# Performance work log

Measured on AMD Instinct MI355X. Metric: run time of the kernel, lower is better.

Reference implementation:

```python
import jax, jax.numpy as jnp
import numpy as np

H = 512  # hidden_dim


def setup_inputs() -> dict:
    key = jax.random.key(0)
    k1, k2, k3 = jax.random.split(key, 3)
    context = jax.random.normal(k1, (32, 512, H), dtype=jnp.float32)
    query = jax.random.normal(k2, (32, 64, H), dtype=jnp.float32)
    # similarity_linear.weight has shape (1, 3H); store flattened as (3H,)
    W = jax.random.normal(k3, (3 * H,), dtype=jnp.float32) * (1.0 / np.sqrt(3 * H))
    return {"context": context, "query": query, "W": W}


def reference(context, query, W):
    # Decompose W into the three blocks applied to [c, q, c*q].
    w_c, w_q, w_m = W[:H], W[H:2 * H], W[2 * H:]
    # S[b,i,j] = c_i.w_c + q_j.w_q + sum_d c_id * q_jd * w_m_d  -- same math as
    # Linear(3H,1) over cat([c_exp, q_exp, c_exp*q_exp]), without the O(B*C*Q*3H) tensor.
    s_c = context @ w_c                       # [B, C]
    s_q = query @ w_q                         # [B, Q]
    s_m = jnp.einsum('bcd,bqd->bcq', context * w_m, query)  # [B, C, Q]
    S = s_m + s_c[:, :, None] + s_q[:, None, :]              # [B, C, Q]

    a = jax.nn.softmax(S, axis=2)             # context-to-query attention
    attended_query = jnp.einsum('bcq,bqd->bcd', a, query)    # [B, C, H]

    b = jax.nn.softmax(jnp.max(S, axis=2), axis=1)           # [B, C]
    attended_context = jnp.einsum('bc,bcd->bd', b, context)  # [B, H]
    attended_context = jnp.broadcast_to(attended_context[:, None, :], context.shape)

    G = jnp.concatenate([
        context,
        attended_query,
        context * attended_query,
        context * attended_context,
    ], axis=2)  # [B, C, 4H]
    return G
```

## Files before the change

kernel.cpp:

```cpp
#include <hip/hip_runtime.h>
#include <cstdint>

#define NB 32
#define NC 512
#define NQ 64
#define ND 512

typedef __attribute__((ext_vector_type(8))) short bf16x8;
typedef __attribute__((ext_vector_type(8))) short short8;
typedef __attribute__((ext_vector_type(4))) float f32x4;

__device__ __forceinline__ short f2bf(float f) {
  union { float f; unsigned u; } v; v.f = f;
  v.u += 0x7fffu + ((v.u >> 16) & 1u);
  return (short)(v.u >> 16);
}

#define PITCH 72
#define P_OFF  0
#define CM_OFF 4608
#define QQ_OFF 9216
#define SCS_F  6912
#define SQS_F  6976
#define PML_F  7040
#define PEL_F  7168
#define AQF_F  7296
#define AQP    68
#define SM_SHORTS 23296

__device__ __forceinline__ int qswz(int dd) {
  return (((dd & 7) ^ ((dd >> 3) & 7)) * 8);
}

__global__ __launch_bounds__(512) void k1_main(
    const float* __restrict__ ctx, const float* __restrict__ qry,
    const float* __restrict__ W, float* __restrict__ G, float* __restrict__ m_ws)
{
  __shared__ __align__(16) short sm[SM_SHORTS];
  float* smf = (float*)sm;

  const int t    = threadIdx.x;
  const int lane = t & 63;
  const int w    = t >> 6;
  const int ln15 = lane & 15;
  const int g    = lane >> 4;
  const int cw   = (w >> 1) * 16;
  const int qh   = w & 1;
  const int qw   = qh * 32;
  const int b    = blockIdx.x >> 3;
  const int c0   = (blockIdx.x & 7) * 64;

  const int lr = t >> 3;
  const int j8 = (t & 7) * 8;

  f32x4 acc[2] = {};
  float scp = 0.f, sqp = 0.f;

  for (int kc = 0; kc < 8; ++kc) {
    const int d0 = kc * 64;
    __syncthreads();
    {
      const float* crow = ctx + ((size_t)(b*NC + c0 + lr))*ND + d0 + j8;
      const float4 ca = *(const float4*)(crow);
      const float4 cb = *(const float4*)(crow + 4);
      const float4 wca = *(const float4*)(W + d0 + j8);
      const float4 wcb = *(const float4*)(W + d0 + j8 + 4);
      const float4 wma = *(const float4*)(W + 2*ND + d0 + j8);
      const float4 wmb = *(const float4*)(W + 2*ND + d0 + j8 + 4);
      scp += ca.x*wca.x + ca.y*wca.y + ca.z*wca.z + ca.w*wca.w
           + cb.x*wcb.x + cb.y*wcb.y + cb.z*wcb.z + cb.w*wcb.w;
      short8 cs;
      cs[0]=f2bf(ca.x*wma.x); cs[1]=f2bf(ca.y*wma.y); cs[2]=f2bf(ca.z*wma.z); cs[3]=f2bf(ca.w*wma.w);
      cs[4]=f2bf(cb.x*wmb.x); cs[5]=f2bf(cb.y*wmb.y); cs[6]=f2bf(cb.z*wmb.z); cs[7]=f2bf(cb.w*wmb.w);
      *(short8*)&sm[CM_OFF + lr*PITCH + j8] = cs;
    }
    {
      const float* qrow = qry + ((size_t)(b*NQ + lr))*ND + d0 + j8;
      const float4 qa = *(const float4*)(qrow);
      const float4 qb = *(const float4*)(qrow + 4);
      const float4 wqa = *(const float4*)(W + ND + d0 + j8);
      const float4 wqb = *(const float4*)(W + ND + d0 + j8 + 4);
      sqp += qa.x*wqa.x + qa.y*wqa.y + qa.z*wqa.z + qa.w*wqa.w
           + qb.x*wqb.x + qb.y*wqb.y + qb.z*wqb.z + qb.w*wqb.w;
      short8 qs;
      qs[0]=f2bf(qa.x); qs[1]=f2bf(qa.y); qs[2]=f2bf(qa.z); qs[3]=f2bf(qa.w);
      qs[4]=f2bf(qb.x); qs[5]=f2bf(qb.y); qs[6]=f2bf(qb.z); qs[7]=f2bf(qb.w);
      *(short8*)&sm[QQ_OFF + lr*PITCH + j8] = qs;
    }
    __syncthreads();
    #pragma unroll
    for (int kk = 0; kk < 2; ++kk) {
      const bf16x8 a = *(const bf16x8*)&sm[CM_OFF + (cw + ln15)*PITCH + kk*32 + g*8];
      #pragma unroll
      for (int n = 0; n < 2; ++n) {
        const bf16x8 bq = *(const bf16x8*)&sm[QQ_OFF + (qw + n*16 + ln15)*PITCH + kk*32 + g*8];
        acc[n] = __builtin_amdgcn_mfma_f32_16x16x32_bf16(a, bq, acc[n], 0, 0, 0);
      }
    }
  }

  scp += __shfl_xor(scp, 1, 8); scp += __shfl_xor(scp, 2, 8); scp += __shfl_xor(scp, 4, 8);
  sqp += __shfl_xor(sqp, 1, 8); sqp += __shfl_xor(sqp, 2, 8); sqp += __shfl_xor(sqp, 4, 8);
  if ((t & 7) == 0) { smf[SCS_F + lr] = scp; smf[SQS_F + lr] = sqp; }
  __syncthreads();

  float ev0[4], ev1[4], pmr[4];
  #pragma unroll
  for (int reg = 0; reg < 4; ++reg) {
    float sv0 = acc[0][reg] + smf[SQS_F + qw + ln15];
    float sv1 = acc[1][reg] + smf[SQS_F + qw + 16 + ln15];
    float pm = fmaxf(sv0, sv1);
    pm = fmaxf(pm, __shfl_xor(pm, 1, 16));
    pm = fmaxf(pm, __shfl_xor(pm, 2, 16));
    pm = fmaxf(pm, __shfl_xor(pm, 4, 16));
    pm = fmaxf(pm, __shfl_xor(pm, 8, 16));
    const float e0 = __expf(sv0 - pm), e1 = __expf(sv1 - pm);
    float pe = e0 + e1;
    pe += __shfl_xor(pe, 1, 16); pe += __shfl_xor(pe, 2, 16);
    pe += __shfl_xor(pe, 4, 16); pe += __shfl_xor(pe, 8, 16);
    ev0[reg] = e0; ev1[reg] = e1; pmr[reg] = pm;
    if (ln15 == 0) { smf[PML_F + qh*64 + cw + g*4 + reg] = pm;
                     smf[PEL_F + qh*64 + cw + g*4 + reg] = pe; }
  }
  __syncthreads();

  #pragma unroll
  for (int reg = 0; reg < 4; ++reg) {
    const int rloc = cw + g*4 + reg;
    const float m0 = smf[PML_F + rloc], m1 = smf[PML_F + 64 + rloc];
    const float s0 = smf[PEL_F + rloc], s1 = smf[PEL_F + 64 + rloc];
    const float M  = fmaxf(m0, m1);
    const float S  = s0*__expf(m0 - M) + s1*__expf(m1 - M);
    const float f  = __expf(pmr[reg] - M) / S;
    if (qh == 0 && ln15 == 0) m_ws[b*NC + c0 + rloc] = M + smf[SCS_F + rloc];
    sm[P_OFF + rloc*PITCH + qw + ln15]      = f2bf(ev0[reg] * f);
    sm[P_OFF + rloc*PITCH + qw + 16 + ln15] = f2bf(ev1[reg] * f);
  }
  __syncthreads();

  bf16x8 pa[2];
  pa[0] = *(const bf16x8*)&sm[P_OFF + (cw + ln15)*PITCH + g*8];
  pa[1] = *(const bf16x8*)&sm[P_OFF + (cw + ln15)*PITCH + 32 + g*8];

  const int sr = t >> 4, sc = (t & 15) * 4;

  for (int dc = 0; dc < 8; ++dc) {
    const int d0 = dc * 64;
    __syncthreads();
    {
      const float* qrow = qry + ((size_t)(b*NQ + lr))*ND + d0 + j8;
      const float4 a0 = *(const float4*)(qrow);
      const float4 a1 = *(const float4*)(qrow + 4);
      const float e[8] = {a0.x,a0.y,a0.z,a0.w,a1.x,a1.y,a1.z,a1.w};
      #pragma unroll
      for (int v = 0; v < 8; ++v) {
        const int dd = j8 + v;
        sm[CM_OFF + dd*PITCH + (lr ^ qswz(dd))] = f2bf(e[v]);
      }
    }
    __syncthreads();
    f32x4 acc2[2] = {};
    #pragma unroll
    for (int kk = 0; kk < 2; ++kk)
      #pragma unroll
      for (int n = 0; n < 2; ++n) {
        const int dd = qw + n*16 + ln15;
        const bf16x8 bq = *(const bf16x8*)&sm[CM_OFF + dd*PITCH + ((kk*32 + g*8) ^ qswz(dd))];
        acc2[n] = __builtin_amdgcn_mfma_f32_16x16x32_bf16(pa[kk], bq, acc2[n], 0, 0, 0);
      }
    #pragma unroll
    for (int n = 0; n < 2; ++n)
      #pragma unroll
      for (int reg = 0; reg < 4; ++reg)
        smf[AQF_F + (cw + g*4 + reg)*AQP + qw + n*16 + ln15] = acc2[n][reg];
    __syncthreads();
    #pragma unroll
    for (int k4 = 0; k4 < 2; ++k4) {
      const int r = k4*32 + sr;
      const float4 aq4 = *(const float4*)&smf[AQF_F + r*AQP + sc];
      const float4 cv  = *(const float4*)(ctx + ((size_t)(b*NC + c0 + r))*ND + d0 + sc);
      float* gp = G + ((size_t)(b*NC + c0 + r))*2048 + d0 + sc;
      *(float4*)(gp)        = cv;
      *(float4*)(gp + 512)  = aq4;
      *(float4*)(gp + 1024) = make_float4(cv.x*aq4.x, cv.y*aq4.y,
                                          cv.z*aq4.z, cv.w*aq4.w);
    }
  }
}

__global__ __launch_bounds__(256) void k2_partial(
    const float* __restrict__ ctx, const float* __restrict__ m_ws, float* __restrict__ pc)
{
  const int t  = threadIdx.x;
  const int b  = blockIdx.x >> 4;
  const int ch = blockIdx.x & 15;
  __shared__ float r8[8];
  __shared__ float wts[32];

  const float v0 = m_ws[b*NC + t];
  const float v1 = m_ws[b*NC + 256 + t];
  float mx = fmaxf(v0, v1);
  #pragma unroll
  for (int o = 32; o; o >>= 1) mx = fmaxf(mx, __shfl_xor(mx, o, 64));
  if ((t & 63) == 0) r8[t >> 6] = mx;
  __syncthreads();
  mx = fmaxf(fmaxf(r8[0], r8[1]), fmaxf(r8[2], r8[3]));
  float e = __expf(v0 - mx) + __expf(v1 - mx);
  #pragma unroll
  for (int o = 32; o; o >>= 1) e += __shfl_xor(e, o, 64);
  if ((t & 63) == 0) r8[4 + (t >> 6)] = e;
  __syncthreads();
  const float denom = r8[4] + r8[5] + r8[6] + r8[7];
  if (t < 32) wts[t] = __expf(m_ws[b*NC + ch*32 + t] - mx) / denom;
  __syncthreads();

  float s0 = 0.f, s1 = 0.f;
  const float* base = ctx + ((size_t)(b*NC + ch*32))*ND;
  for (int c = 0; c < 32; ++c) {
    const float w = wts[c];
    s0 += w * base[(size_t)c*ND + t];
    s1 += w * base[(size_t)c*ND + t + 256];
  }
  pc[((size_t)(b*16 + ch))*ND + t]       = s0;
  pc[((size_t)(b*16 + ch))*ND + t + 256] = s1;
}

__global__ __launch_bounds__(512) void k2_reduce(
    const float* __restrict__ pc, float* __restrict__ ac)
{
  const int b = blockIdx.x;
  const int d = threadIdx.x;
  float s = 0.f;
  #pragma unroll
  for (int ch = 0; ch < 16; ++ch) s += pc[((size_t)(b*16 + ch))*ND + d];
  ac[b*ND + d] = s;
}

__global__ __launch_bounds__(256) void k3_part3(
    const float* __restrict__ ctx, const float* __restrict__ ac, float* __restrict__ G)
{
  const size_t e = ((size_t)blockIdx.x*256 + threadIdx.x) * 8;
  const int b = (int)(e >> 18);
  const int r = (int)(e & 262143);
  const int c = r >> 9;
  const int d = r & 511;
  const float4 x0 = *(const float4*)(ctx + e);
  const float4 x1 = *(const float4*)(ctx + e + 4);
  const float4 a0 = *(const float4*)(ac + b*ND + d);
  const float4 a1 = *(const float4*)(ac + b*ND + d + 4);
  float* gp = G + ((size_t)(b*NC + c))*2048 + 1536 + d;
  *(float4*)(gp)     = make_float4(x0.x*a0.x, x0.y*a0.y, x0.z*a0.z, x0.w*a0.w);
  *(float4*)(gp + 4) = make_float4(x1.x*a1.x, x1.y*a1.y, x1.z*a1.z, x1.w*a1.w);
}

extern "C" void kernel_launch(void* const* d_in, const int* in_sizes, int n_in,
                              void* d_out, int out_size, void* d_ws, size_t ws_size,
                              hipStream_t stream)
{
  const float* ctx = (const float*)d_in[0];
  const float* qry = (const float*)d_in[1];
  const float* W   = (const float*)d_in[2];
  float* G = (float*)d_out;

  float* m_ws = (float*)d_ws;
  float* pc   = m_ws + NB*NC;
  float* ac   = pc + (size_t)NB*16*ND;

  k1_main   <<<dim3(NB*8),  dim3(512), 0, stream>>>(ctx, qry, W, G, m_ws);
  k2_partial<<<dim3(NB*16), dim3(256), 0, stream>>>(ctx, m_ws, pc);
  k2_reduce <<<dim3(NB),    dim3(512), 0, stream>>>(pc, ac);
  k3_part3  <<<dim3((NB*NC*ND)/(256*8)), dim3(256), 0, stream>>>(ctx, ac, G);
}
```

Before: 65.00 us.

## Widen d-chunks to 128, write context slice early, store attended query as bf16

The chunk width in both the score loop and the attended-query loop doubles from 64 to 128, which halves the number of iterations and barriers. The block index is swizzled across batches. The first G slice (context copy) is now written during the score phase from the context values already loaded. The attended-query staging buffer in shared memory becomes bf16, so the epilogue reads fewer bytes and G's attended-query part now carries bf16 precision. This cuts synchronization and duplicate global context loads for the copy, but adds precision loss and register pressure.

```diff
diff --git a/kernel.cpp b/kernel.cpp
--- a/kernel.cpp
+++ b/kernel.cpp
@@ -15,17 +15,20 @@
   v.u += 0x7fffu + ((v.u >> 16) & 1u);
   return (short)(v.u >> 16);
 }
-
-#define PITCH 72
-#define P_OFF  0
-#define CM_OFF 4608
-#define QQ_OFF 9216
-#define SCS_F  6912
-#define SQS_F  6976
-#define PML_F  7040
-#define PEL_F  7168
-#define AQF_F  7296
-#define AQP    68
+__device__ __forceinline__ float bf2f(short s) {
+  union { float f; unsigned u; } v; v.u = ((unsigned)(unsigned short)s) << 16;
+  return v.f;
+}
+
+#define P_OFF   0
+#define CM_OFF  4608
+#define QQ_OFF  13312
+#define QT_OFF  4608
+#define AQB_OFF 13824
+#define SCS_F   11264
+#define SQS_F   11328
+#define PML_F   11392
+#define PEL_F   11520
 #define SM_SHORTS 23296
 
 __device__ __forceinline__ int qswz(int dd) {
@@ -47,53 +50,74 @@
   const int cw   = (w >> 1) * 16;
   const int qh   = w & 1;
   const int qw   = qh * 32;
-  const int b    = blockIdx.x >> 3;
-  const int c0   = (blockIdx.x & 7) * 64;
-
-  const int lr = t >> 3;
-  const int j8 = (t & 7) * 8;
+  const int bid  = (int)blockIdx.x;
+  const int swz  = (bid & 7) * 32 + (bid >> 3);
+  const int b    = swz >> 3;
+  const int c0   = (swz & 7) * 64;
+
+  const int lr  = t >> 3;
+  const int j16 = (t & 7) * 16;
 
   f32x4 acc[2] = {};
   float scp = 0.f, sqp = 0.f;
 
-  for (int kc = 0; kc < 8; ++kc) {
-    const int d0 = kc * 64;
+  for (int kc = 0; kc < 4; ++kc) {
+    const int d0 = kc * 128;
     __syncthreads();
     {
-      const float* crow = ctx + ((size_t)(b*NC + c0 + lr))*ND + d0 + j8;
-      const float4 ca = *(const float4*)(crow);
-      const float4 cb = *(const float4*)(crow + 4);
-      const float4 wca = *(const float4*)(W + d0 + j8);
-      const float4 wcb = *(const float4*)(W + d0 + j8 + 4);
-      const float4 wma = *(const float4*)(W + 2*ND + d0 + j8);
-      const float4 wmb = *(const float4*)(W + 2*ND + d0 + j8 + 4);
-      scp += ca.x*wca.x + ca.y*wca.y + ca.z*wca.z + ca.w*wca.w
-           + cb.x*wcb.x + cb.y*wcb.y + cb.z*wcb.z + cb.w*wcb.w;
-      short8 cs;
-      cs[0]=f2bf(ca.x*wma.x); cs[1]=f2bf(ca.y*wma.y); cs[2]=f2bf(ca.z*wma.z); cs[3]=f2bf(ca.w*wma.w);
-      cs[4]=f2bf(cb.x*wmb.x); cs[5]=f2bf(cb.y*wmb.y); cs[6]=f2bf(cb.z*wmb.z); cs[7]=f2bf(cb.w*wmb.w);
-      *(short8*)&sm[CM_OFF + lr*PITCH + j8] = cs;
+      const float* crow = ctx + ((size_t)(b*NC + c0 + lr))*ND + d0 + j16;
+      float4 cv0 = ((const float4*)crow)[0], cv1 = ((const float4*)crow)[1];
+      float4 cv2 = ((const float4*)crow)[2], cv3 = ((const float4*)crow)[3];
+      const float4 wc0 = *(const float4*)(W + d0 + j16);
+      const float4 wc1 = *(const float4*)(W + d0 + j16 + 4);
+      const float4 wc2 = *(const float4*)(W + d0 + j16 + 8);
+      const float4 wc3 = *(const float4*)(W + d0 + j16 + 12);
+      const float4 wm0 = *(const float4*)(W + 2*ND + d0 + j16);
+      const float4 wm1 = *(const float4*)(W + 2*ND + d0 + j16 + 4);
+      const float4 wm2 = *(const float4*)(W + 2*ND + d0 + j16 + 8);
+      const float4 wm3 = *(const float4*)(W + 2*ND + d0 + j16 + 12);
+      scp += cv0.x*wc0.x + cv0.y*wc0.y + cv0.z*wc0.z + cv0.w*wc0.w
+           + cv1.x*wc1.x + cv1.y*wc1.y + cv1.z*wc1.z + cv1.w*wc1.w
+           + cv2.x*wc2.x + cv2.y*wc2.y + cv2.z*wc2.z + cv2.w*wc2.w
+           + cv3.x*wc3.x + cv3.y*wc3.y + cv3.z*wc3.z + cv3.w*wc3.w;
+      short8 s0, s1;
+      s0[0]=f2bf(cv0.x*wm0.x); s0[1]=f2bf(cv0.y*wm0.y); s0[2]=f2bf(cv0.z*wm0.z); s0[3]=f2bf(cv0.w*wm0.w);
+      s0[4]=f2bf(cv1.x*wm1.x); s0[5]=f2bf(cv1.y*wm1.y); s0[6]=f2bf(cv1.z*wm1.z); s0[7]=f2bf(cv1.w*wm1.w);
+      s1[0]=f2bf(cv2.x*wm2.x); s1[1]=f2bf(cv2.y*wm2.y); s1[2]=f2bf(cv2.z*wm2.z); s1[3]=f2bf(cv2.w*wm2.w);
+      s1[4]=f2bf(cv3.x*wm3.x); s1[5]=f2bf(cv3.y*wm3.y); s1[6]=f2bf(cv3.z*wm3.z); s1[7]=f2bf(cv3.w*wm3.w);
+      *(short8*)&sm[CM_OFF + lr*136 + j16]     = s0;
+      *(short8*)&sm[CM_OFF + lr*136 + j16 + 8] = s1;
+      float* gp0 = G + ((size_t)(b*NC + c0 + lr))*2048 + d0 + j16;
+      ((float4*)gp0)[0] = cv0; ((float4*)gp0)[1] = cv1;
+      ((float4*)gp0)[2] = cv2; ((float4*)gp0)[3] = cv3;
     }
     {
-      const float* qrow = qry + ((size_t)(b*NQ + lr))*ND + d0 + j8;
-      const float4 qa = *(const float4*)(qrow);
-      const float4 qb = *(const float4*)(qrow + 4);
-      const float4 wqa = *(const float4*)(W + ND + d0 + j8);
-      const float4 wqb = *(const float4*)(W + ND + d0 + j8 + 4);
-      sqp += qa.x*wqa.x + qa.y*wqa.y + qa.z*wqa.z + qa.w*wqa.w
-           + qb.x*wqb.x + qb.y*wqb.y + qb.z*wqb.z + qb.w*wqb.w;
-      short8 qs;
-      qs[0]=f2bf(qa.x); qs[1]=f2bf(qa.y); qs[2]=f2bf(qa.z); qs[3]=f2bf(qa.w);
-      qs[4]=f2bf(qb.x); qs[5]=f2bf(qb.y); qs[6]=f2bf(qb.z); qs[7]=f2bf(qb.w);
-      *(short8*)&sm[QQ_OFF + lr*PITCH + j8] = qs;
+      const float* qrow = qry + ((size_t)(b*NQ + lr))*ND + d0 + j16;
+      float4 qv0 = ((const float4*)qrow)[0], qv1 = ((const float4*)qrow)[1];
+      float4 qv2 = ((const float4*)qrow)[2], qv3 = ((const float4*)qrow)[3];
+      const float4 wq0 = *(const float4*)(W + ND + d0 + j16);
+      const float4 wq1 = *(const float4*)(W + ND + d0 + j16 + 4);
+      const float4 wq2 = *(const float4*)(W + ND + d0 + j16 + 8);
+      const float4 wq3 = *(const float4*)(W + ND + d0 + j16 + 12);
+      sqp += qv0.x*wq0.x + qv0.y*wq0.y + qv0.z*wq0.z + qv0.w*wq0.w
+           + qv1.x*wq1.x + qv1.y*wq1.y + qv1.z*wq1.z + qv1.w*wq1.w
+           + qv2.x*wq2.x + qv2.y*wq2.y + qv2.z*wq2.z + qv2.w*wq2.w
+           + qv3.x*wq3.x + qv3.y*wq3.y + qv3.z*wq3.z + qv3.w*wq3.w;
+      short8 s0, s1;
+      s0[0]=f2bf(qv0.x); s0[1]=f2bf(qv0.y); s0[2]=f2bf(qv0.z); s0[3]=f2bf(qv0.w);
+      s0[4]=f2bf(qv1.x); s0[5]=f2bf(qv1.y); s0[6]=f2bf(qv1.z); s0[7]=f2bf(qv1.w);
+      s1[0]=f2bf(qv2.x); s1[1]=f2bf(qv2.y); s1[2]=f2bf(qv2.z); s1[3]=f2bf(qv2.w);
+      s1[4]=f2bf(qv3.x); s1[5]=f2bf(qv3.y); s1[6]=f2bf(qv3.z); s1[7]=f2bf(qv3.w);
+      *(short8*)&sm[QQ_OFF + lr*136 + j16]     = s0;
+      *(short8*)&sm[QQ_OFF + lr*136 + j16 + 8] = s1;
     }
     __syncthreads();
     #pragma unroll
-    for (int kk = 0; kk < 2; ++kk) {
-      const bf16x8 a = *(const bf16x8*)&sm[CM_OFF + (cw + ln15)*PITCH + kk*32 + g*8];
+    for (int kk = 0; kk < 4; ++kk) {
+      const bf16x8 a = *(const bf16x8*)&sm[CM_OFF + (cw + ln15)*136 + kk*32 + g*8];
       #pragma unroll
       for (int n = 0; n < 2; ++n) {
-        const bf16x8 bq = *(const bf16x8*)&sm[QQ_OFF + (qw + n*16 + ln15)*PITCH + kk*32 + g*8];
+        const bf16x8 bq = *(const bf16x8*)&sm[QQ_OFF + (qw + n*16 + ln15)*136 + kk*32 + g*8];
         acc[n] = __builtin_amdgcn_mfma_f32_16x16x32_bf16(a, bq, acc[n], 0, 0, 0);
       }
     }
@@ -133,57 +157,68 @@
     const float S  = s0*__expf(m0 - M) + s1*__expf(m1 - M);
     const float f  = __expf(pmr[reg] - M) / S;
     if (qh == 0 && ln15 == 0) m_ws[b*NC + c0 + rloc] = M + smf[SCS_F + rloc];
-    sm[P_OFF + rloc*PITCH + qw + ln15]      = f2bf(ev0[reg] * f);
-    sm[P_OFF + rloc*PITCH + qw + 16 + ln15] = f2bf(ev1[reg] * f);
+    sm[P_OFF + rloc*72 + qw + ln15]      = f2bf(ev0[reg] * f);
+    sm[P_OFF + rloc*72 + qw + 16 + ln15] = f2bf(ev1[reg] * f);
   }
   __syncthreads();
 
   bf16x8 pa[2];
-  pa[0] = *(const bf16x8*)&sm[P_OFF + (cw + ln15)*PITCH + g*8];
-  pa[1] = *(const bf16x8*)&sm[P_OFF + (cw + ln15)*PITCH + 32 + g*8];
-
-  const int sr = t >> 4, sc = (t & 15) * 4;
-
-  for (int dc = 0; dc < 8; ++dc) {
-    const int d0 = dc * 64;
+  pa[0] = *(const bf16x8*)&sm[P_OFF + (cw + ln15)*72 + g*8];
+  pa[1] = *(const bf16x8*)&sm[P_OFF + (cw + ln15)*72 + 32 + g*8];
+
+  const int dh = qh;
+
+  for (int dc = 0; dc < 4; ++dc) {
+    const int d0 = dc * 128;
     __syncthreads();
     {
-      const float* qrow = qry + ((size_t)(b*NQ + lr))*ND + d0 + j8;
-      const float4 a0 = *(const float4*)(qrow);
-      const float4 a1 = *(const float4*)(qrow + 4);
-      const float e[8] = {a0.x,a0.y,a0.z,a0.w,a1.x,a1.y,a1.z,a1.w};
-      #pragma unroll
-      for (int v = 0; v < 8; ++v) {
-        const int dd = j8 + v;
-        sm[CM_OFF + dd*PITCH + (lr ^ qswz(dd))] = f2bf(e[v]);
+      const float* qrow = qry + ((size_t)(b*NQ + lr))*ND + d0 + j16;
+      const float4 a0 = ((const float4*)qrow)[0];
+      const float4 a1 = ((const float4*)qrow)[1];
+      const float4 a2 = ((const float4*)qrow)[2];
+      const float4 a3 = ((const float4*)qrow)[3];
+      const float e[16] = {a0.x,a0.y,a0.z,a0.w, a1.x,a1.y,a1.z,a1.w,
+                           a2.x,a2.y,a2.z,a2.w, a3.x,a3.y,a3.z,a3.w};
+      #pragma unroll
+      for (int v = 0; v < 16; ++v) {
+        const int dd = j16 + v;
+        sm[QT_OFF + dd*72 + (lr ^ qswz(dd))] = f2bf(e[v]);
       }
     }
     __syncthreads();
-    f32x4 acc2[2] = {};
+    f32x4 acc2[4] = {};
     #pragma unroll
     for (int kk = 0; kk < 2; ++kk)
       #pragma unroll
-      for (int n = 0; n < 2; ++n) {
-        const int dd = qw + n*16 + ln15;
-        const bf16x8 bq = *(const bf16x8*)&sm[CM_OFF + dd*PITCH + ((kk*32 + g*8) ^ qswz(dd))];
+      for (int n = 0; n < 4; ++n) {
+        const int dd = dh*64 + n*16 + ln15;
+        const bf16x8 bq = *(const bf16x8*)&sm[QT_OFF + dd*72 + ((kk*32 + g*8) ^ qswz(dd))];
         acc2[n] = __builtin_amdgcn_mfma_f32_16x16x32_bf16(pa[kk], bq, acc2[n], 0, 0, 0);
       }
     #pragma unroll
-    for (int n = 0; n < 2; ++n)
+    for (int n = 0; n < 4; ++n)
       #pragma unroll
       for (int reg = 0; reg < 4; ++reg)
-        smf[AQF_F + (cw + g*4 + reg)*AQP + qw + n*16 + ln15] = acc2[n][reg];
-    __syncthreads();
-    #pragma unroll
-    for (int k4 = 0; k4 < 2; ++k4) {
-      const int r = k4*32 + sr;
-      const float4 aq4 = *(const float4*)&smf[AQF_F + r*AQP + sc];
-      const float4 cv  = *(const float4*)(ctx + ((size_t)(b*NC + c0 + r))*ND + d0 + sc);
-      float* gp = G + ((size_t)(b*NC + c0 + r))*2048 + d0 + sc;
-      *(float4*)(gp)        = cv;
-      *(float4*)(gp + 512)  = aq4;
-      *(float4*)(gp + 1024) = make_float4(cv.x*aq4.x, cv.y*aq4.y,
-                                          cv.z*aq4.z, cv.w*aq4.w);
+        sm[AQB_OFF + (cw + g*4 + reg)*136 + dh*64 + n*16 + ln15] = f2bf(acc2[n][reg]);
+    __syncthreads();
+    {
+      const short8 ab0 = *(const short8*)&sm[AQB_OFF + lr*136 + j16];
+      const short8 ab1 = *(const short8*)&sm[AQB_OFF + lr*136 + j16 + 8];
+      float aq[16];
+      #pragma unroll
+      for (int i = 0; i < 8; ++i) { aq[i] = bf2f(ab0[i]); aq[8+i] = bf2f(ab1[i]); }
+      const float* crow = ctx + ((size_t)(b*NC + c0 + lr))*ND + d0 + j16;
+      float4 cv0 = ((const float4*)crow)[0], cv1 = ((const float4*)crow)[1];
+      float4 cv2 = ((const float4*)crow)[2], cv3 = ((const float4*)crow)[3];
+      float* gp = G + ((size_t)(b*NC + c0 + lr))*2048 + d0 + j16;
+      ((float4*)(gp + 512))[0] = make_float4(aq[0], aq[1], aq[2], aq[3]);
+      ((float4*)(gp + 512))[1] = make_float4(aq[4], aq[5], aq[6], aq[7]);
+      ((float4*)(gp + 512))[2] = make_float4(aq[8], aq[9], aq[10], aq[11]);
+      ((float4*)(gp + 512))[3] = make_float4(aq[12], aq[13], aq[14], aq[15]);
+      ((float4*)(gp + 1024))[0] = make_float4(cv0.x*aq[0], cv0.y*aq[1], cv0.z*aq[2], cv0.w*aq[3]);
+      ((float4*)(gp + 1024))[1] = make_float4(cv1.x*aq[4], cv1.y*aq[5], cv1.z*aq[6], cv1.w*aq[7]);
+      ((float4*)(gp + 1024))[2] = make_float4(cv2.x*aq[8], cv2.y*aq[9], cv2.z*aq[10], cv2.w*aq[11]);
+      ((float4*)(gp + 1024))[3] = make_float4(cv3.x*aq[12], cv3.y*aq[13], cv3.z*aq[14], cv3.w*aq[15]);
     }
   }
 }
```

After: 79.99 us. +23.1%, slower.

## Split score/softmax from output pass, fuse all four G blocks in one kernel

Applied to the files above, without the earlier changes.

Restructures the pipeline so one kernel computes scores and the softmax probabilities and writes them in bf16 to workspace. A prep kernel transposes query to bf16 once per batch, and a new output kernel does the P·Q matmul and writes all four G segments in one pass. This removes the separate part-3 kernel, which re-read context, and the per-chunk query transpose inside the main loop. It adds the round-trips for P and transposed Q, and rounds attended_query to bf16 before storing, which loses precision. Kernel A and kernel B each use 256 threads and 32 context rows per block.

```diff
diff --git a/kernel.cpp b/kernel.cpp
--- a/kernel.cpp
+++ b/kernel.cpp
@@ -15,28 +15,54 @@
   v.u += 0x7fffu + ((v.u >> 16) & 1u);
   return (short)(v.u >> 16);
 }
-
-#define PITCH 72
-#define P_OFF  0
-#define CM_OFF 4608
-#define QQ_OFF 9216
-#define SCS_F  6912
-#define SQS_F  6976
-#define PML_F  7040
-#define PEL_F  7168
-#define AQF_F  7296
-#define AQP    68
-#define SM_SHORTS 23296
-
-__device__ __forceinline__ int qswz(int dd) {
-  return (((dd & 7) ^ ((dd >> 3) & 7)) * 8);
-}
-
-__global__ __launch_bounds__(512) void k1_main(
+__device__ __forceinline__ float bf2f(short s) {
+  union { float f; unsigned u; } v; v.u = ((unsigned)(unsigned short)s) << 16;
+  return v.f;
+}
+
+__global__ __launch_bounds__(512) void kPrep(
+    const float* __restrict__ qry, short* __restrict__ qTbf)
+{
+  __shared__ short lq[NQ*ND];
+  const int b = blockIdx.x;
+  const int t = threadIdx.x;
+  const int r = t >> 3;
+  const int cb = (t & 7) * 64;
+  const float* qrow = qry + ((size_t)(b*NQ + r))*ND + cb;
+  #pragma unroll
+  for (int i = 0; i < 16; ++i) {
+    const float4 qv = *(const float4*)(qrow + i*4);
+    short4 s; s.x=f2bf(qv.x); s.y=f2bf(qv.y); s.z=f2bf(qv.z); s.w=f2bf(qv.w);
+    *(short4*)&lq[r*ND + cb + i*4] = s;
+  }
+  __syncthreads();
+  const int d = t;
+  short* qTrow = qTbf + ((size_t)(b*ND + d))*NQ;
+  #pragma unroll
+  for (int j = 0; j < 16; ++j) {
+    short4 h4;
+    h4.x = lq[(j*4+0)*ND + d];
+    h4.y = lq[(j*4+1)*ND + d];
+    h4.z = lq[(j*4+2)*ND + d];
+    h4.w = lq[(j*4+3)*ND + d];
+    *(short4*)&qTrow[j*4] = h4;
+  }
+}
+
+#define KA_CM 0
+#define KA_QQ 2304
+#define KA_P  6912
+#define KA_SCS 4608
+#define KA_SQS 4640
+#define KA_PML 4704
+#define KA_PEL 4768
+#define KA_SHORTS 9664
+
+__global__ __launch_bounds__(256) void kA(
     const float* __restrict__ ctx, const float* __restrict__ qry,
-    const float* __restrict__ W, float* __restrict__ G, float* __restrict__ m_ws)
-{
-  __shared__ __align__(16) short sm[SM_SHORTS];
+    const float* __restrict__ W, short* __restrict__ Pws, float* __restrict__ m_ws)
+{
+  __shared__ __align__(16) short sm[KA_SHORTS];
   float* smf = (float*)sm;
 
   const int t    = threadIdx.x;
@@ -47,11 +73,11 @@
   const int cw   = (w >> 1) * 16;
   const int qh   = w & 1;
   const int qw   = qh * 32;
-  const int b    = blockIdx.x >> 3;
-  const int c0   = (blockIdx.x & 7) * 64;
-
-  const int lr = t >> 3;
-  const int j8 = (t & 7) * 8;
+  const int b    = blockIdx.x >> 4;
+  const int c0   = (blockIdx.x & 15) * 32;
+
+  const int lr = t >> 3, j8  = (t & 7) * 8;
+  const int qr = t >> 2, i16 = (t & 3) * 16;
 
   f32x4 acc[2] = {};
   float scp = 0.f, sqp = 0.f;
@@ -72,43 +98,54 @@
       short8 cs;
       cs[0]=f2bf(ca.x*wma.x); cs[1]=f2bf(ca.y*wma.y); cs[2]=f2bf(ca.z*wma.z); cs[3]=f2bf(ca.w*wma.w);
       cs[4]=f2bf(cb.x*wmb.x); cs[5]=f2bf(cb.y*wmb.y); cs[6]=f2bf(cb.z*wmb.z); cs[7]=f2bf(cb.w*wmb.w);
-      *(short8*)&sm[CM_OFF + lr*PITCH + j8] = cs;
+      *(short8*)&sm[KA_CM + lr*72 + j8] = cs;
     }
     {
-      const float* qrow = qry + ((size_t)(b*NQ + lr))*ND + d0 + j8;
+      const float* qrow = qry + ((size_t)(b*NQ + qr))*ND + d0 + i16;
       const float4 qa = *(const float4*)(qrow);
       const float4 qb = *(const float4*)(qrow + 4);
-      const float4 wqa = *(const float4*)(W + ND + d0 + j8);
-      const float4 wqb = *(const float4*)(W + ND + d0 + j8 + 4);
-      sqp += qa.x*wqa.x + qa.y*wqa.y + qa.z*wqa.z + qa.w*wqa.w
-           + qb.x*wqb.x + qb.y*wqb.y + qb.z*wqb.z + qb.w*wqb.w;
-      short8 qs;
-      qs[0]=f2bf(qa.x); qs[1]=f2bf(qa.y); qs[2]=f2bf(qa.z); qs[3]=f2bf(qa.w);
-      qs[4]=f2bf(qb.x); qs[5]=f2bf(qb.y); qs[6]=f2bf(qb.z); qs[7]=f2bf(qb.w);
-      *(short8*)&sm[QQ_OFF + lr*PITCH + j8] = qs;
+      const float4 qc = *(const float4*)(qrow + 8);
+      const float4 qd = *(const float4*)(qrow + 12);
+      const float4 wa  = *(const float4*)(W + ND + d0 + i16);
+      const float4 wb  = *(const float4*)(W + ND + d0 + i16 + 4);
+      const float4 wc2 = *(const float4*)(W + ND + d0 + i16 + 8);
+      const float4 wd  = *(const float4*)(W + ND + d0 + i16 + 12);
+      sqp += qa.x*wa.x + qa.y*wa.y + qa.z*wa.z + qa.w*wa.w
+           + qb.x*wb.x + qb.y*wb.y + qb.z*wb.z + qb.w*wb.w
+           + qc.x*wc2.x + qc.y*wc2.y + qc.z*wc2.z + qc.w*wc2.w
+           + qd.x*wd.x + qd.y*wd.y + qd.z*wd.z + qd.w*wd.w;
+      short8 s1, s2;
+      s1[0]=f2bf(qa.x); s1[1]=f2bf(qa.y); s1[2]=f2bf(qa.z); s1[3]=f2bf(qa.w);
+      s1[4]=f2bf(qb.x); s1[5]=f2bf(qb.y); s1[6]=f2bf(qb.z); s1[7]=f2bf(qb.w);
+      s2[0]=f2bf(qc.x); s2[1]=f2bf(qc.y); s2[2]=f2bf(qc.z); s2[3]=f2bf(qc.w);
+      s2[4]=f2bf(qd.x); s2[5]=f2bf(qd.y); s2[6]=f2bf(qd.z); s2[7]=f2bf(qd.w);
+      *(short8*)&sm[KA_QQ + qr*72 + i16]     = s1;
+      *(short8*)&sm[KA_QQ + qr*72 + i16 + 8] = s2;
     }
     __syncthreads();
     #pragma unroll
     for (int kk = 0; kk < 2; ++kk) {
-      const bf16x8 a = *(const bf16x8*)&sm[CM_OFF + (cw + ln15)*PITCH + kk*32 + g*8];
+      const bf16x8 a = *(const bf16x8*)&sm[KA_CM + (cw + ln15)*72 + kk*32 + g*8];
       #pragma unroll
       for (int n = 0; n < 2; ++n) {
-        const bf16x8 bq = *(const bf16x8*)&sm[QQ_OFF + (qw + n*16 + ln15)*PITCH + kk*32 + g*8];
+        const bf16x8 bq = *(const bf16x8*)&sm[KA_QQ + (qw + n*16 + ln15)*72 + kk*32 + g*8];
         acc[n] = __builtin_amdgcn_mfma_f32_16x16x32_bf16(a, bq, acc[n], 0, 0, 0);
       }
     }
   }
 
   scp += __shfl_xor(scp, 1, 8); scp += __shfl_xor(scp, 2, 8); scp += __shfl_xor(scp, 4, 8);
-  sqp += __shfl_xor(sqp, 1, 8); sqp += __shfl_xor(sqp, 2, 8); sqp += __shfl_xor(sqp, 4, 8);
-  if ((t & 7) == 0) { smf[SCS_F + lr] = scp; smf[SQS_F + lr] = sqp; }
+  if ((t & 7) == 0) smf[KA_SCS + lr] = scp;
+  sqp += __shfl_xor(sqp, 1, 4); sqp += __shfl_xor(sqp, 2, 4);
+  if ((t & 3) == 0) smf[KA_SQS + qr] = sqp;
   __syncthreads();
 
   float ev0[4], ev1[4], pmr[4];
   #pragma unroll
   for (int reg = 0; reg < 4; ++reg) {
-    float sv0 = acc[0][reg] + smf[SQS_F + qw + ln15];
-    float sv1 = acc[1][reg] + smf[SQS_F + qw + 16 + ln15];
+    const int rloc = cw + g*4 + reg;
+    float sv0 = acc[0][reg] + smf[KA_SQS + qw + ln15];
+    float sv1 = acc[1][reg] + smf[KA_SQS + qw + 16 + ln15];
     float pm = fmaxf(sv0, sv1);
     pm = fmaxf(pm, __shfl_xor(pm, 1, 16));
     pm = fmaxf(pm, __shfl_xor(pm, 2, 16));
@@ -119,72 +156,29 @@
     pe += __shfl_xor(pe, 1, 16); pe += __shfl_xor(pe, 2, 16);
     pe += __shfl_xor(pe, 4, 16); pe += __shfl_xor(pe, 8, 16);
     ev0[reg] = e0; ev1[reg] = e1; pmr[reg] = pm;
-    if (ln15 == 0) { smf[PML_F + qh*64 + cw + g*4 + reg] = pm;
-                     smf[PEL_F + qh*64 + cw + g*4 + reg] = pe; }
+    if (ln15 == 0) { smf[KA_PML + qh*32 + rloc] = pm;
+                     smf[KA_PEL + qh*32 + rloc] = pe; }
   }
   __syncthreads();
 
   #pragma unroll
   for (int reg = 0; reg < 4; ++reg) {
     const int rloc = cw + g*4 + reg;
-    const float m0 = smf[PML_F + rloc], m1 = smf[PML_F + 64 + rloc];
-    const float s0 = smf[PEL_F + rloc], s1 = smf[PEL_F + 64 + rloc];
+    const float m0 = smf[KA_PML + rloc], m1 = smf[KA_PML + 32 + rloc];
+    const float s0 = smf[KA_PEL + rloc], s1 = smf[KA_PEL + 32 + rloc];
     const float M  = fmaxf(m0, m1);
     const float S  = s0*__expf(m0 - M) + s1*__expf(m1 - M);
     const float f  = __expf(pmr[reg] - M) / S;
-    if (qh == 0 && ln15 == 0) m_ws[b*NC + c0 + rloc] = M + smf[SCS_F + rloc];
-    sm[P_OFF + rloc*PITCH + qw + ln15]      = f2bf(ev0[reg] * f);
-    sm[P_OFF + rloc*PITCH + qw + 16 + ln15] = f2bf(ev1[reg] * f);
-  }
-  __syncthreads();
-
-  bf16x8 pa[2];
-  pa[0] = *(const bf16x8*)&sm[P_OFF + (cw + ln15)*PITCH + g*8];
-  pa[1] = *(const bf16x8*)&sm[P_OFF + (cw + ln15)*PITCH + 32 + g*8];
-
-  const int sr = t >> 4, sc = (t & 15) * 4;
-
-  for (int dc = 0; dc < 8; ++dc) {
-    const int d0 = dc * 64;
-    __syncthreads();
-    {
-      const float* qrow = qry + ((size_t)(b*NQ + lr))*ND + d0 + j8;
-      const float4 a0 = *(const float4*)(qrow);
-      const float4 a1 = *(const float4*)(qrow + 4);
-      const float e[8] = {a0.x,a0.y,a0.z,a0.w,a1.x,a1.y,a1.z,a1.w};
-      #pragma unroll
-      for (int v = 0; v < 8; ++v) {
-        const int dd = j8 + v;
-        sm[CM_OFF + dd*PITCH + (lr ^ qswz(dd))] = f2bf(e[v]);
-      }
-    }
-    __syncthreads();
-    f32x4 acc2[2] = {};
-    #pragma unroll
-    for (int kk = 0; kk < 2; ++kk)
-      #pragma unroll
-      for (int n = 0; n < 2; ++n) {
-        const int dd = qw + n*16 + ln15;
-        const bf16x8 bq = *(const bf16x8*)&sm[CM_OFF + dd*PITCH + ((kk*32 + g*8) ^ qswz(dd))];
-        acc2[n] = __builtin_amdgcn_mfma_f32_16x16x32_bf16(pa[kk], bq, acc2[n], 0, 0, 0);
-      }
-    #pragma unroll
-    for (int n = 0; n < 2; ++n)
-      #pragma unroll
-      for (int reg = 0; reg < 4; ++reg)
-        smf[AQF_F + (cw + g*4 + reg)*AQP + qw + n*16 + ln15] = acc2[n][reg];
-    __syncthreads();
-    #pragma unroll
-    for (int k4 = 0; k4 < 2; ++k4) {
-      const int r = k4*32 + sr;
-      const float4 aq4 = *(const float4*)&smf[AQF_F + r*AQP + sc];
-      const float4 cv  = *(const float4*)(ctx + ((size_t)(b*NC + c0 + r))*ND + d0 + sc);
-      float* gp = G + ((size_t)(b*NC + c0 + r))*2048 + d0 + sc;
-      *(float4*)(gp)        = cv;
-      *(float4*)(gp + 512)  = aq4;
-      *(float4*)(gp + 1024) = make_float4(cv.x*aq4.x, cv.y*aq4.y,
-                                          cv.z*aq4.z, cv.w*aq4.w);
-    }
+    if (qh == 0 && ln15 == 0) m_ws[b*NC + c0 + rloc] = M + smf[KA_SCS + rloc];
+    sm[KA_P + rloc*72 + qw + ln15]      = f2bf(ev0[reg] * f);
+    sm[KA_P + rloc*72 + qw + 16 + ln15] = f2bf(ev1[reg] * f);
+  }
+  __syncthreads();
+
+  {
+    const int row = t >> 3, col8 = (t & 7) * 8;
+    const short8 v = *(const short8*)&sm[KA_P + row*72 + col8];
+    *(short8*)&Pws[((size_t)(b*NC + c0 + row))*NQ + col8] = v;
   }
 }
 
@@ -236,21 +230,103 @@
   ac[b*ND + d] = s;
 }
 
-__global__ __launch_bounds__(256) void k3_part3(
-    const float* __restrict__ ctx, const float* __restrict__ ac, float* __restrict__ G)
-{
-  const size_t e = ((size_t)blockIdx.x*256 + threadIdx.x) * 8;
-  const int b = (int)(e >> 18);
-  const int r = (int)(e & 262143);
-  const int c = r >> 9;
-  const int d = r & 511;
-  const float4 x0 = *(const float4*)(ctx + e);
-  const float4 x1 = *(const float4*)(ctx + e + 4);
-  const float4 a0 = *(const float4*)(ac + b*ND + d);
-  const float4 a1 = *(const float4*)(ac + b*ND + d + 4);
-  float* gp = G + ((size_t)(b*NC + c))*2048 + 1536 + d;
-  *(float4*)(gp)     = make_float4(x0.x*a0.x, x0.y*a0.y, x0.z*a0.z, x0.w*a0.w);
-  *(float4*)(gp + 4) = make_float4(x1.x*a1.x, x1.y*a1.y, x1.z*a1.z, x1.w*a1.w);
+#define KB_QT 0
+#define KB_P  18432
+#define KB_AQ 20736
+#define KB_ACF 14976
+#define KB_SHORTS 30976
+
+__global__ __launch_bounds__(256) void kB(
+    const float* __restrict__ ctx, const short* __restrict__ qTbf,
+    const short* __restrict__ Pws, const float* __restrict__ ac,
+    float* __restrict__ G)
+{
+  __shared__ __align__(16) short sm[KB_SHORTS];
+  float* smf = (float*)sm;
+
+  const int t    = threadIdx.x;
+  const int lane = t & 63;
+  const int w    = t >> 6;
+  const int ln15 = lane & 15;
+  const int g    = lane >> 4;
+  const int b    = blockIdx.x >> 4;
+  const int c0   = (blockIdx.x & 15) * 32;
+
+  {
+    const int row = t >> 3, col8 = (t & 7) * 8;
+    *(short8*)&sm[KB_P + row*72 + col8] =
+        *(const short8*)&Pws[((size_t)(b*NC + c0 + row))*NQ + col8];
+  }
+  smf[KB_ACF + t]       = ac[b*ND + t];
+  smf[KB_ACF + 256 + t] = ac[b*ND + 256 + t];
+  {
+    const int rr = t >> 3, col8 = (t & 7) * 8;
+    #pragma unroll
+    for (int ii = 0; ii < 8; ++ii) {
+      const int dd = ii*32 + rr;
+      *(short8*)&sm[KB_QT + dd*72 + col8] =
+          *(const short8*)&qTbf[((size_t)(b*ND + dd))*NQ + col8];
+    }
+  }
+  __syncthreads();
+
+  bf16x8 pa[2][2];
+  #pragma unroll
+  for (int cf = 0; cf < 2; ++cf)
+    #pragma unroll
+    for (int kk = 0; kk < 2; ++kk)
+      pa[cf][kk] = *(const bf16x8*)&sm[KB_P + (cf*16 + ln15)*72 + kk*32 + g*8];
+
+  #pragma unroll
+  for (int h = 0; h < 2; ++h) {
+    f32x4 acc2[2][4] = {};
+    #pragma unroll
+    for (int kk = 0; kk < 2; ++kk)
+      #pragma unroll
+      for (int n = 0; n < 4; ++n) {
+        const int dd = w*64 + n*16 + ln15;
+        const bf16x8 bq = *(const bf16x8*)&sm[KB_QT + dd*72 + kk*32 + g*8];
+        acc2[0][n] = __builtin_amdgcn_mfma_f32_16x16x32_bf16(pa[0][kk], bq, acc2[0][n], 0, 0, 0);
+        acc2[1][n] = __builtin_amdgcn_mfma_f32_16x16x32_bf16(pa[1][kk], bq, acc2[1][n], 0, 0, 0);
+      }
+    #pragma unroll
+    for (int cf = 0; cf < 2; ++cf)
+      #pragma unroll
+      for (int n = 0; n < 4; ++n)
+        #pragma unroll
+        for (int reg = 0; reg < 4; ++reg)
+          sm[KB_AQ + w*2304 + (cf*16 + g*4 + reg)*72 + n*16 + ln15] = f2bf(acc2[cf][n][reg]);
+    __syncthreads();
+
+    if (h == 0) {
+      const int rr = t >> 3, col8 = (t & 7) * 8;
+      #pragma unroll
+      for (int ii = 0; ii < 8; ++ii) {
+        const int dd = ii*32 + rr;
+        *(short8*)&sm[KB_QT + dd*72 + col8] =
+            *(const short8*)&qTbf[((size_t)(b*ND + 256 + dd))*NQ + col8];
+      }
+    }
+
+    #pragma unroll
+    for (int i = 0; i < 8; ++i) {
+      const int task = i*16 + (t >> 4);
+      const int r  = task & 31;
+      const int sg = task >> 5;
+      const int dglob = h*256 + sg*64 + (t & 15)*4;
+      const short4 a4 = *(const short4*)&sm[KB_AQ + sg*2304 + r*72 + (t & 15)*4];
+      const float4 cv = *(const float4*)(ctx + ((size_t)(b*NC + c0 + r))*ND + dglob);
+      const float4 acv = *(const float4*)&smf[KB_ACF + dglob];
+      const float q0 = bf2f(a4.x), q1 = bf2f(a4.y), q2 = bf2f(a4.z), q3 = bf2f(a4.w);
+      float* gp = G + ((size_t)(b*NC + c0 + r))*2048 + dglob;
+      *(float4*)(gp)        = cv;
+      *(float4*)(gp + 512)  = make_float4(q0, q1, q2, q3);
+      *(float4*)(gp + 1024) = make_float4(cv.x*q0, cv.y*q1, cv.z*q2, cv.w*q3);
+      *(float4*)(gp + 1536) = make_float4(cv.x*acv.x, cv.y*acv.y,
+                                          cv.z*acv.z, cv.w*acv.w);
+    }
+    if (h == 0) __syncthreads();
+  }
 }
 
 extern "C" void kernel_launch(void* const* d_in, const int* in_sizes, int n_in,
@@ -262,12 +338,16 @@
   const float* W   = (const float*)d_in[2];
   float* G = (float*)d_out;
 
-  float* m_ws = (float*)d_ws;
-  float* pc   = m_ws + NB*NC;
-  float* ac   = pc + (size_t)NB*16*ND;
-
-  k1_main   <<<dim3(NB*8),  dim3(512), 0, stream>>>(ctx, qry, W, G, m_ws);
+  float* ws   = (float*)d_ws;
+  float* m_ws = ws;
+  float* pc   = ws + 16384;
+  float* ac   = ws + 278528;
+  short* qTbf = (short*)(ws + 294912);
+  short* Pws  = qTbf + (size_t)NB*ND*NQ;
+
+  kPrep     <<<dim3(NB),    dim3(512), 0, stream>>>(qry, qTbf);
+  kA        <<<dim3(NB*16), dim3(256), 0, stream>>>(ctx, qry, W, Pws, m_ws);
   k2_partial<<<dim3(NB*16), dim3(256), 0, stream>>>(ctx, m_ws, pc);
   k2_reduce <<<dim3(NB),    dim3(512), 0, stream>>>(pc, ac);
-  k3_part3  <<<dim3((NB*NC*ND)/(256*8)), dim3(256), 0, stream>>>(ctx, ac, G);
-}
+  kB        <<<dim3(NB*16), dim3(256), 0, stream>>>(ctx, qTbf, Pws, ac, G);
+}
```

Measured after the change: 64.41 us. No clear change (-0.9%).
